# Optimization experiments

Hardware: AMD Instinct MI355X
Metric: run time of the kernel (lower is better)

The kernel has to match this reference:

```python
import jax, jax.numpy as jnp
import numpy as np
from jax import lax

B, W, K = 64, 128, 64      # batch, window_size, n_features
KS = 7                      # conv kernel size
EF = W                      # feature-attn embed dim (defaults to window_size, GATv1)
ET = 2 * K                  # temporal-attn embed dim (n_features doubled by GATv2)
H = 256                     # GRU hidden
FH = 256                    # forecast MLP hidden
ALPHA = 0.2                 # leaky relu slope


def _leaky(v):
    return jnp.where(v >= 0, v, ALPHA * v)


def setup_inputs() -> dict:
    key = jax.random.key(0)
    ks = jax.random.split(key, 20)
    s = 0.05
    inp = {
        "x": jax.random.normal(ks[0], (B, W, K), jnp.float32),
        # ConvLayer
        "conv_w": jax.random.normal(ks[1], (K, K, KS), jnp.float32) * s,
        "conv_b": jnp.zeros((K,), jnp.float32),
        # FeatureAttentionLayer (GATv1): lin W->EF, a:[2EF,1], bias [K,K]
        "feat_lin_w": jax.random.normal(ks[2], (EF, W), jnp.float32) * s,
        "feat_lin_b": jnp.zeros((EF,), jnp.float32),
        "feat_a": jax.random.normal(ks[3], (2 * EF, 1), jnp.float32) * s,
        "feat_bias": jnp.zeros((K, K), jnp.float32),
        # TemporalAttentionLayer (GATv2): lin 2K->ET, a:[ET,1], bias [W,W]
        "temp_lin_w": jax.random.normal(ks[4], (ET, 2 * K), jnp.float32) * s,
        "temp_lin_b": jnp.zeros((ET,), jnp.float32),
        "temp_a": jax.random.normal(ks[5], (ET, 1), jnp.float32) * s,
        "temp_bias": jnp.zeros((W, W), jnp.float32),
        # GRU (1 layer), input dim 3K
        "gru_wih": jax.random.normal(ks[6], (3 * H, 3 * K), jnp.float32) * s,
        "gru_whh": jax.random.normal(ks[7], (3 * H, H), jnp.float32) * s,
        "gru_bih": jnp.zeros((3 * H,), jnp.float32),
        "gru_bhh": jnp.zeros((3 * H,), jnp.float32),
        "fc0_w": jax.random.normal(ks[8], (FH, H), jnp.float32) * s,
        "fc0_b": jnp.zeros((FH,), jnp.float32),
        "fc1_w": jax.random.normal(ks[9], (FH, FH), jnp.float32) * s,
        "fc1_b": jnp.zeros((FH,), jnp.float32),
        "fc2_w": jax.random.normal(ks[10], (FH, FH), jnp.float32) * s,
        "fc2_b": jnp.zeros((FH,), jnp.float32),
        "fc3_w": jax.random.normal(ks[11], (K, FH), jnp.float32) * s,
        "fc3_b": jnp.zeros((K,), jnp.float32),
    }
    return inp


def _forward(x, conv_w, conv_b, feat_lin_w, feat_lin_b, feat_a, feat_bias,
             temp_lin_w, temp_lin_b, temp_a, temp_bias,
             gru_wih, gru_whh, gru_bih, gru_bhh,
             fc0_w, fc0_b, fc1_w, fc1_b, fc2_w, fc2_b, fc3_w, fc3_b):
    # --- ConvLayer: pad (k-1)//2 both sides, Conv1d K->K, ReLU ---
    pad = (KS - 1) // 2
    xc = x.transpose(0, 2, 1)                                   # [B,K,W]
    xc = jnp.pad(xc, ((0, 0), (0, 0), (pad, pad)))
    y = lax.conv_general_dilated(xc, conv_w, (1,), 'VALID',
                                 dimension_numbers=('NCH', 'OIH', 'NCH'))
    y = jax.nn.relu(y + conv_b[None, :, None]).transpose(0, 2, 1)  # [B,W,K]

    # --- FeatureAttentionLayer (GATv1): e_ij = leaky((Wx_i||Wx_j)·a) ---
    xf = y.transpose(0, 2, 1)                                   # [B,K,W]
    Wx = xf @ feat_lin_w.T + feat_lin_b                         # [B,K,EF]
    s1 = Wx @ feat_a[:EF, 0]                                    # [B,K]
    s2 = Wx @ feat_a[EF:, 0]                                    # [B,K]
    e_f = _leaky(s1[:, :, None] + s2[:, None, :]) + feat_bias   # [B,K,K]
    att_f = jax.nn.softmax(e_f, axis=2)
    h_feat = jax.nn.sigmoid(att_f @ xf).transpose(0, 2, 1)      # [B,W,K]

    # --- TemporalAttentionLayer (GATv2): g = leaky(lin(x_i||x_j)); e = g·a ---
    W1, W2 = temp_lin_w[:, :K], temp_lin_w[:, K:]               # split lin over concat halves
    p = y @ W1.T                                                # [B,W,ET]
    q = y @ W2.T                                                # [B,W,ET]
    g = _leaky(p[:, :, None, :] + q[:, None, :, :] + temp_lin_b)  # [B,W,W,ET]
    e_t = (g @ temp_a)[..., 0] + temp_bias                      # [B,W,W]
    att_t = jax.nn.softmax(e_t, axis=2)
    h_temp = jax.nn.sigmoid(att_t @ y)                          # [B,W,K]

    # --- concat + GRU over time ---
    z = jnp.concatenate([y, h_feat, h_temp], axis=2)            # [B,W,3K]

    def gru_step(h, xt):
        gi = xt @ gru_wih.T + gru_bih                           # [B,3H]
        gh = h @ gru_whh.T + gru_bhh
        ir, iz, inn = jnp.split(gi, 3, axis=1)
        hr, hz, hn = jnp.split(gh, 3, axis=1)
        r = jax.nn.sigmoid(ir + hr)
        zg = jax.nn.sigmoid(iz + hz)
        n = jnp.tanh(inn + r * hn)
        return (1.0 - zg) * n + zg * h, None

    h0 = jnp.zeros((z.shape[0], H), z.dtype)
    h_end, _ = lax.scan(gru_step, h0, z.transpose(1, 0, 2))     # [B,H]

    # --- Forecasting MLP (eval mode: dropout is identity) ---
    v = jax.nn.relu(h_end @ fc0_w.T + fc0_b)
    v = jax.nn.relu(v @ fc1_w.T + fc1_b)
    v = jax.nn.relu(v @ fc2_w.T + fc2_b)
    return v @ fc3_w.T + fc3_b                                  # [B,K]


def reference(x, conv_w, conv_b, feat_lin_w, feat_lin_b, feat_a, feat_bias,
              temp_lin_w, temp_lin_b, temp_a, temp_bias,
              gru_wih, gru_whh, gru_bih, gru_bhh,
              fc0_w, fc0_b, fc1_w, fc1_b, fc2_w, fc2_b, fc3_w, fc3_b):
    return _forward(x, conv_w, conv_b, feat_lin_w, feat_lin_b, feat_a, feat_bias,
                    temp_lin_w, temp_lin_b, temp_a, temp_bias,
                    gru_wih, gru_whh, gru_bih, gru_bhh,
                    fc0_w, fc0_b, fc1_w, fc1_b, fc2_w, fc2_b, fc3_w, fc3_b)
```

## Files before the change

### kernel.cpp

```cpp
#include <hip/hip_runtime.h>
#include <hip/hip_bf16.h>

typedef unsigned int uint;
typedef _Float16 half2_t __attribute__((ext_vector_type(2)));

union H2U { uint u; half2_t h; };

#if defined(__has_builtin)
#if __has_builtin(__builtin_amdgcn_fdot2)
#define HAVE_FDOT2 1
#endif
#endif

__device__ __forceinline__ float dot2acc(uint w, uint hh, float acc) {
    H2U a; a.u = w; H2U b; b.u = hh;
#ifdef HAVE_FDOT2
    return __builtin_amdgcn_fdot2(a.h, b.h, acc, false);
#else
    return acc + (float)a.h.x * (float)b.h.x + (float)a.h.y * (float)b.h.y;
#endif
}

#define OFF_Y    0u
#define OFF_Z    524288u
#define OFF_GI   2097152u
#define OFF_WHH  8388608u
#define OFF_C12  8486912u
#define OFF_DD   8487168u
#define OFF_HEND 8487424u

__global__ void k_prep(const float* __restrict__ flw, const float* __restrict__ flb,
                       const float* __restrict__ fa, float* __restrict__ c12,
                       float* __restrict__ dd) {
    int tid = threadIdx.x;
    float a = 0.f, b = 0.f;
    for (int e = 0; e < 128; ++e) {
        float w = flw[e * 128 + tid];
        a = fmaf(w, fa[e], a);
        b = fmaf(w, fa[128 + e], b);
    }
    c12[tid] = a;
    c12[128 + tid] = b;
    if (tid == 0) {
        float d1 = 0.f, d2 = 0.f;
        for (int e = 0; e < 128; ++e) { d1 += flb[e] * fa[e]; d2 += flb[e] * fa[128 + e]; }
        dd[0] = d1; dd[1] = d2;
    }
}

__global__ __launch_bounds__(256) void k_pack(const float* __restrict__ whh, uint* __restrict__ w16) {
    int idx = blockIdx.x * 256 + threadIdx.x;
    if (idx >= 98304) return;
    int tidq = idx >> 7;
    int r7 = idx & 127;
    int rowpar = r7 >> 6;
    int i = r7 & 63;
    int half = tidq / 384;
    int m = tidq % 384;
    int row = 2 * m + rowpar;
    int pc = half * 64 + i;
    float a = whh[(size_t)row * 256 + 2 * pc];
    float b = whh[(size_t)row * 256 + 2 * pc + 1];
    H2U u; u.h.x = (_Float16)a; u.h.y = (_Float16)b;
    w16[idx] = u.u;
}

__global__ __launch_bounds__(256) void k_conv(const float* __restrict__ x, const float* __restrict__ cw,
                                              const float* __restrict__ cb, float* __restrict__ y,
                                              float* __restrict__ z) {
    __shared__ float xT[64][41];
    __shared__ float cwL[64 * 64 * 7];
    int b = blockIdx.y, w0 = blockIdx.x * 32, tid = threadIdx.x;
    for (int idx = tid; idx < 38 * 64; idx += 256) {
        int wl = idx / 64, k = idx % 64;
        int wg = w0 - 3 + wl;
        xT[k][wl] = (wg >= 0 && wg < 128) ? x[((size_t)b * 128 + wg) * 64 + k] : 0.f;
    }
    for (int idx = tid; idx < 64 * 64 * 7; idx += 256) cwL[idx] = cw[idx];
    __syncthreads();
    int w_l = tid % 32, kog = tid / 32;
    float acc[8];
#pragma unroll
    for (int i = 0; i < 8; ++i) acc[i] = 0.f;
    for (int ki = 0; ki < 64; ++ki) {
        float x7[7];
#pragma unroll
        for (int u = 0; u < 7; ++u) x7[u] = xT[ki][w_l + u];
#pragma unroll
        for (int koi = 0; koi < 8; ++koi) {
            const float* wp = &cwL[((kog * 8 + koi) * 64 + ki) * 7];
#pragma unroll
            for (int u = 0; u < 7; ++u) acc[koi] = fmaf(x7[u], wp[u], acc[koi]);
        }
    }
    int w = w0 + w_l;
#pragma unroll
    for (int koi = 0; koi < 8; ++koi) {
        int ko = kog * 8 + koi;
        float v = acc[koi] + cb[ko];
        v = v > 0.f ? v : 0.f;
        y[((size_t)b * 128 + w) * 64 + ko] = v;
        z[((size_t)b * 128 + w) * 192 + ko] = v;
    }
}

__global__ __launch_bounds__(256) void k_feat(const float* __restrict__ y, const float* __restrict__ c12,
                                              const float* __restrict__ dd, const float* __restrict__ fb,
                                              float* __restrict__ z) {
    int b = blockIdx.y, w0 = blockIdx.x * 32, tid = threadIdx.x;
    __shared__ float s1L[64], s2L[64];
    __shared__ float attL[64][65];
    __shared__ float yL[32][64];
    __shared__ float cL[256];
    cL[tid] = c12[tid];
    for (int idx = tid; idx < 32 * 64; idx += 256) {
        int wl = idx / 64, j = idx % 64;
        yL[wl][j] = y[((size_t)b * 128 + w0 + wl) * 64 + j];
    }
    __syncthreads();
    if (tid < 128) {
        int k = tid % 64;
        const float* c = (tid < 64) ? cL : cL + 128;
        float acc = 0.f;
        for (int w = 0; w < 128; ++w) acc = fmaf(y[((size_t)b * 128 + w) * 64 + k], c[w], acc);
        if (tid < 64) s1L[k] = acc + dd[0]; else s2L[k] = acc + dd[1];
    }
    __syncthreads();
    if (tid < 64) {
        int k = tid;
        float s1 = s1L[k];
        float m = -1e30f;
        for (int j = 0; j < 64; ++j) {
            float v = s1 + s2L[j];
            float l = fmaxf(v, 0.2f * v);
            float e = l + fb[k * 64 + j];
            attL[k][j] = e;
            m = fmaxf(m, e);
        }
        float s = 0.f;
        for (int j = 0; j < 64; ++j) { float e = __expf(attL[k][j] - m); attL[k][j] = e; s += e; }
        float inv = 1.f / s;
        for (int j = 0; j < 64; ++j) attL[k][j] *= inv;
    }
    __syncthreads();
    int k_l = tid % 64, wg = tid / 64;
    for (int wi = 0; wi < 8; ++wi) {
        int wl = wg * 8 + wi;
        float acc = 0.f;
#pragma unroll 16
        for (int j = 0; j < 64; ++j) acc = fmaf(attL[k_l][j], yL[wl][j], acc);
        float hv = 1.f / (1.f + __expf(-acc));
        z[((size_t)b * 128 + w0 + wl) * 192 + 64 + k_l] = hv;
    }
}

__global__ __launch_bounds__(512) void k_temp(const float* __restrict__ y, const float* __restrict__ tlw,
                                              const float* __restrict__ tlb, const float* __restrict__ ta,
                                              const float* __restrict__ tbias, float* __restrict__ z) {
    int b = blockIdx.y, i0 = blockIdx.x * 32, tid = threadIdx.x;
    __shared__ __align__(16) float yT[64][132];
    __shared__ __align__(16) float qL[128][128];
    __shared__ __align__(16) float pL[32][128];
    __shared__ __align__(16) float etL[32][128];
    __shared__ __align__(16) float taL[128];
    __shared__ float mred[32][8], sred[32][8];
    __shared__ float mrow[32], invL[32];
    if (tid < 128) taL[tid] = ta[tid];
    for (int idx = tid; idx < 8192; idx += 512) {
        int j = idx >> 6, k = idx & 63;
        yT[k][j] = y[((size_t)b * 128 + j) * 64 + k];
    }
    __syncthreads();
    {
        int c = tid & 127, ih = tid >> 7;
        float w1r[64];
        const float4* w1p = (const float4*)(tlw + c * 128);
#pragma unroll
        for (int q4 = 0; q4 < 16; ++q4) {
            float4 v = w1p[q4];
            w1r[4 * q4] = v.x; w1r[4 * q4 + 1] = v.y; w1r[4 * q4 + 2] = v.z; w1r[4 * q4 + 3] = v.w;
        }
        float base = tlb[c];
#pragma unroll
        for (int ilb = 0; ilb < 2; ++ilb) {
            int j0 = i0 + ih * 8 + ilb * 4;
            float4 acc = {base, base, base, base};
            for (int k = 0; k < 64; ++k) {
                float4 yv = *((const float4*)&yT[k][j0]);
                float w = w1r[k];
                acc.x = fmaf(yv.x, w, acc.x); acc.y = fmaf(yv.y, w, acc.y);
                acc.z = fmaf(yv.z, w, acc.z); acc.w = fmaf(yv.w, w, acc.w);
            }
            int il = ih * 8 + ilb * 4;
            pL[il][c] = acc.x; pL[il + 1][c] = acc.y; pL[il + 2][c] = acc.z; pL[il + 3][c] = acc.w;
        }
    }
    {
        int j = tid & 127, ch = tid >> 7;
        float yreg[64];
#pragma unroll
        for (int k = 0; k < 64; ++k) yreg[k] = yT[k][j];
        for (int cc = 0; cc < 32; ++cc) {
            int c = __builtin_amdgcn_readfirstlane(ch * 32 + cc);
            const float* w2 = tlw + c * 128 + 64;
            float acc = 0.f;
#pragma unroll
            for (int k = 0; k < 64; ++k) acc = fmaf(yreg[k], w2[k], acc);
            qL[c][j] = acc;
        }
    }
    __syncthreads();
    {
        int jg = tid & 31, ih = tid >> 5;
        int j0 = jg * 4;
        int il0 = ih * 2;
        float4 acc0 = *((const float4*)(tbias + (size_t)(i0 + il0) * 128 + j0));
        float4 acc1 = *((const float4*)(tbias + (size_t)(i0 + il0 + 1) * 128 + j0));
        for (int c0 = 0; c0 < 128; c0 += 4) {
            float4 ta4 = *((const float4*)&taL[c0]);
            float4 p0 = *((const float4*)&pL[il0][c0]);
            float4 p1 = *((const float4*)&pL[il0 + 1][c0]);
            float4 q0 = *((const float4*)&qL[c0 + 0][j0]);
            float4 q1 = *((const float4*)&qL[c0 + 1][j0]);
            float4 q2 = *((const float4*)&qL[c0 + 2][j0]);
            float4 q3 = *((const float4*)&qL[c0 + 3][j0]);
#define ETSTEP(qv, tac, pa, pb) { \
            float u; \
            u = (pa) + qv.x; acc0.x = fmaf(fmaxf(u, 0.2f * u), (tac), acc0.x); \
            u = (pa) + qv.y; acc0.y = fmaf(fmaxf(u, 0.2f * u), (tac), acc0.y); \
            u = (pa) + qv.z; acc0.z = fmaf(fmaxf(u, 0.2f * u), (tac), acc0.z); \
            u = (pa) + qv.w; acc0.w = fmaf(fmaxf(u, 0.2f * u), (tac), acc0.w); \
            u = (pb) + qv.x; acc1.x = fmaf(fmaxf(u, 0.2f * u), (tac), acc1.x); \
            u = (pb) + qv.y; acc1.y = fmaf(fmaxf(u, 0.2f * u), (tac), acc1.y); \
            u = (pb) + qv.z; acc1.z = fmaf(fmaxf(u, 0.2f * u), (tac), acc1.z); \
            u = (pb) + qv.w; acc1.w = fmaf(fmaxf(u, 0.2f * u), (tac), acc1.w); }
            ETSTEP(q0, ta4.x, p0.x, p1.x)
            ETSTEP(q1, ta4.y, p0.y, p1.y)
            ETSTEP(q2, ta4.z, p0.z, p1.z)
            ETSTEP(q3, ta4.w, p0.w, p1.w)
#undef ETSTEP
        }
        *((float4*)&etL[il0][j0]) = acc0;
        *((float4*)&etL[il0 + 1][j0]) = acc1;
    }
    __syncthreads();
    if (tid < 256) {
        int il = tid >> 3, seg = tid & 7;
        const float4* ep = (const float4*)&etL[il][seg * 16];
        float m = -1e30f;
#pragma unroll
        for (int q = 0; q < 4; ++q) {
            float4 e = ep[q];
            m = fmaxf(m, fmaxf(fmaxf(e.x, e.y), fmaxf(e.z, e.w)));
        }
        mred[il][seg] = m;
    }
    __syncthreads();
    if (tid < 32) {
        float m = mred[tid][0];
#pragma unroll
        for (int s = 1; s < 8; ++s) m = fmaxf(m, mred[tid][s]);
        mrow[tid] = m;
    }
    __syncthreads();
    if (tid < 256) {
        int il = tid >> 3, seg = tid & 7;
        float m = mrow[il];
        float4* ep = (float4*)&etL[il][seg * 16];
        float s = 0.f;
#pragma unroll
        for (int q = 0; q < 4; ++q) {
            float4 e = ep[q];
            e.x = __expf(e.x - m); e.y = __expf(e.y - m);
            e.z = __expf(e.z - m); e.w = __expf(e.w - m);
            s += (e.x + e.y) + (e.z + e.w);
            ep[q] = e;
        }
        sred[il][seg] = s;
    }
    __syncthreads();
    if (tid < 32) {
        float s = 0.f;
#pragma unroll
        for (int q = 0; q < 8; ++q) s += sred[tid][q];
        invL[tid] = 1.f / s;
    }
    __syncthreads();
    {
        int k = tid & 63, ig = tid >> 6;
        float acc[4] = {0.f, 0.f, 0.f, 0.f};
        const float* yb = y + (size_t)b * 128 * 64 + k;
        for (int j0 = 0; j0 < 128; j0 += 4) {
            float yv[4];
#pragma unroll
            for (int jj = 0; jj < 4; ++jj) yv[jj] = yb[(size_t)(j0 + jj) * 64];
#pragma unroll
            for (int ii = 0; ii < 4; ++ii) {
                int il = ig * 4 + ii;
                float4 ev = *((const float4*)&etL[il][j0]);
                acc[ii] = fmaf(ev.x, yv[0], acc[ii]);
                acc[ii] = fmaf(ev.y, yv[1], acc[ii]);
                acc[ii] = fmaf(ev.z, yv[2], acc[ii]);
                acc[ii] = fmaf(ev.w, yv[3], acc[ii]);
            }
        }
#pragma unroll
        for (int ii = 0; ii < 4; ++ii) {
            int il = ig * 4 + ii;
            float hv = 1.f / (1.f + __expf(-acc[ii] * invL[il]));
            z[((size_t)b * 128 + i0 + il) * 192 + 128 + k] = hv;
        }
    }
}

__global__ __launch_bounds__(256) void k_gi(const float* __restrict__ z, const float* __restrict__ wih,
                                            const float* __restrict__ bih, float* __restrict__ gi) {
    int o0 = blockIdx.x * 128;
    int bt0 = blockIdx.y * 64;
    int tid = threadIdx.x;
    int o_l = tid % 128, rg = tid / 128;
    __shared__ float zL[64][64];
    __shared__ float wT[64][133];
    float acc[32];
#pragma unroll
    for (int r = 0; r < 32; ++r) acc[r] = 0.f;
    for (int mc = 0; mc < 3; ++mc) {
        int m0 = mc * 64;
        __syncthreads();
        for (int idx = tid; idx < 64 * 64; idx += 256) {
            int r = idx / 64, mm = idx % 64;
            zL[r][mm] = z[(size_t)(bt0 + r) * 192 + m0 + mm];
        }
        for (int idx = tid; idx < 128 * 64; idx += 256) {
            int o = idx / 64, mm = idx % 64;
            wT[mm][o] = wih[(size_t)(o0 + o) * 192 + m0 + mm];
        }
        __syncthreads();
        for (int mm = 0; mm < 64; ++mm) {
            float w = wT[mm][o_l];
#pragma unroll
            for (int r = 0; r < 32; ++r) acc[r] = fmaf(zL[rg * 32 + r][mm], w, acc[r]);
        }
    }
    float bo = bih[o0 + o_l];
#pragma unroll
    for (int r = 0; r < 32; ++r)
        gi[(size_t)(bt0 + rg * 32 + r) * 768 + o0 + o_l] = acc[r] + bo;
}

__global__ __launch_bounds__(768, 3) void k_gru(const float* __restrict__ gi,
                                                const uint* __restrict__ w16,
                                                const float* __restrict__ bhh,
                                                float* __restrict__ hend) {
    int b = blockIdx.x, tid = threadIdx.x;
    int m = tid % 384, half = tid / 384;
    int t = tid & 255;
    __shared__ __align__(16) uint4 hp4s[32];
    __shared__ float sH[2][768];
    uint4 wv[32];
    {
        const uint4* wp = (const uint4*)(w16 + (size_t)tid * 128);
#pragma unroll
        for (int i = 0; i < 32; ++i) wv[i] = wp[i];
    }
    float br = 0.f, bz = 0.f, bn = 0.f;
    if (tid < 256) { br = bhh[t]; bz = bhh[256 + t]; bn = bhh[512 + t]; }
    float h = 0.f;
    if (tid < 32) { uint4 zz; zz.x = zz.y = zz.z = zz.w = 0u; hp4s[tid] = zz; }
    __syncthreads();
    const float* gib = gi + (size_t)b * 128 * 768;
    const uint4* hbase = hp4s + half * 16;
    for (int s = 0; s < 128; ++s) {
        float gr = 0.f, gz = 0.f, gn = 0.f;
        if (tid < 256) {
            gr = gib[s * 768 + t];
            gz = gib[s * 768 + 256 + t];
            gn = gib[s * 768 + 512 + t];
        }
        float a0 = 0.f, a1 = 0.f, c0 = 0.f, c1 = 0.f;
#pragma unroll
        for (int j = 0; j < 16; ++j) {
            uint4 hv = hbase[j];
            uint4 wa = wv[j];
            uint4 wb = wv[16 + j];
            a0 = dot2acc(wa.x, hv.x, a0); a1 = dot2acc(wa.y, hv.y, a1);
            a0 = dot2acc(wa.z, hv.z, a0); a1 = dot2acc(wa.w, hv.w, a1);
            c0 = dot2acc(wb.x, hv.x, c0); c1 = dot2acc(wb.y, hv.y, c1);
            c0 = dot2acc(wb.z, hv.z, c0); c1 = dot2acc(wb.w, hv.w, c1);
        }
        float2 pr; pr.x = a0 + a1; pr.y = c0 + c1;
        *((float2*)&sH[half][2 * m]) = pr;
        __syncthreads();
        if (tid < 256) {
            float hr = sH[0][t] + sH[1][t] + br;
            float hz = sH[0][256 + t] + sH[1][256 + t] + bz;
            float hn = sH[0][512 + t] + sH[1][512 + t] + bn;
            float r  = 1.f / (1.f + __expf(-(gr + hr)));
            float zg = 1.f / (1.f + __expf(-(gz + hz)));
            float nx = gn + r * hn;
            float n  = 1.f - 2.f / (1.f + __expf(2.f * nx));
            h = (1.f - zg) * n + zg * h;
            ((_Float16*)hp4s)[t] = (_Float16)h;
        }
        __syncthreads();
    }
    if (tid < 256) hend[b * 256 + t] = h;
}

__global__ __launch_bounds__(256) void k_fc(const float* __restrict__ hend,
                                            const float* __restrict__ w0, const float* __restrict__ b0,
                                            const float* __restrict__ w1, const float* __restrict__ b1,
                                            const float* __restrict__ w2, const float* __restrict__ b2,
                                            const float* __restrict__ w3, const float* __restrict__ b3,
                                            float* __restrict__ out) {
    int b = blockIdx.x, tid = threadIdx.x;
    __shared__ float bufA[256], bufB[256];
    bufA[tid] = hend[b * 256 + tid];
    __syncthreads();
    {
        float acc = b0[tid];
        const float* wrow = &w0[tid * 256];
#pragma unroll 8
        for (int m = 0; m < 256; ++m) acc = fmaf(wrow[m], bufA[m], acc);
        bufB[tid] = fmaxf(acc, 0.f);
    }
    __syncthreads();
    {
        float acc = b1[tid];
        const float* wrow = &w1[tid * 256];
#pragma unroll 8
        for (int m = 0; m < 256; ++m) acc = fmaf(wrow[m], bufB[m], acc);
        bufA[tid] = fmaxf(acc, 0.f);
    }
    __syncthreads();
    {
        float acc = b2[tid];
        const float* wrow = &w2[tid * 256];
#pragma unroll 8
        for (int m = 0; m < 256; ++m) acc = fmaf(wrow[m], bufA[m], acc);
        bufB[tid] = fmaxf(acc, 0.f);
    }
    __syncthreads();
    if (tid < 64) {
        float acc = b3[tid];
        const float* wrow = &w3[tid * 256];
#pragma unroll 8
        for (int m = 0; m < 256; ++m) acc = fmaf(wrow[m], bufB[m], acc);
        out[b * 64 + tid] = acc;
    }
}

extern "C" void kernel_launch(void* const* d_in, const int* in_sizes, int n_in,
                              void* d_out, int out_size, void* d_ws, size_t ws_size,
                              hipStream_t stream) {
    const float* x    = (const float*)d_in[0];
    const float* cw   = (const float*)d_in[1];
    const float* cb   = (const float*)d_in[2];
    const float* flw  = (const float*)d_in[3];
    const float* flb  = (const float*)d_in[4];
    const float* fa   = (const float*)d_in[5];
    const float* fb   = (const float*)d_in[6];
    const float* tlw  = (const float*)d_in[7];
    const float* tlb  = (const float*)d_in[8];
    const float* ta   = (const float*)d_in[9];
    const float* tb   = (const float*)d_in[10];
    const float* wih  = (const float*)d_in[11];
    const float* whh  = (const float*)d_in[12];
    const float* bih  = (const float*)d_in[13];
    const float* bhh  = (const float*)d_in[14];
    const float* fc0w = (const float*)d_in[15];
    const float* fc0b = (const float*)d_in[16];
    const float* fc1w = (const float*)d_in[17];
    const float* fc1b = (const float*)d_in[18];
    const float* fc2w = (const float*)d_in[19];
    const float* fc2b = (const float*)d_in[20];
    const float* fc3w = (const float*)d_in[21];
    const float* fc3b = (const float*)d_in[22];

    float* wsf  = (float*)d_ws;
    float* y    = wsf + OFF_Y;
    float* z    = wsf + OFF_Z;
    float* gi   = wsf + OFF_GI;
    uint*  w16  = (uint*)(wsf + OFF_WHH);
    float* c12  = wsf + OFF_C12;
    float* dd   = wsf + OFF_DD;
    float* hend = wsf + OFF_HEND;
    float* out  = (float*)d_out;

    k_prep<<<1, 128, 0, stream>>>(flw, flb, fa, c12, dd);
    k_pack<<<384, 256, 0, stream>>>(whh, w16);
    k_conv<<<dim3(4, 64), 256, 0, stream>>>(x, cw, cb, y, z);
    k_feat<<<dim3(4, 64), 256, 0, stream>>>(y, c12, dd, fb, z);
    k_temp<<<dim3(4, 64), 512, 0, stream>>>(y, tlw, tlb, ta, tb, z);
    k_gi<<<dim3(6, 128), 256, 0, stream>>>(z, wih, bih, gi);
    k_gru<<<64, 768, 0, stream>>>(gi, w16, bhh, hend);
    k_fc<<<64, 256, 0, stream>>>(hend, fc0w, fc0b, fc1w, fc1b, fc2w, fc2b, fc3w, fc3b, out);
}
```

Before: 459.6 us.

## Restructure GRU to 512 threads with 3 rows each, register-tile gi GEMM, merge prep

The GRU recurrence kernel now uses 512 threads per block, each holding three rows of fp16-packed W_hh in registers (pinned with empty asm constraints), instead of 768 threads with two rows each. This cuts the number of waves taking part in each per-step barrier and gives every hidden-state LDS read more reuse. The input-gate GEMM is rewritten as an 8x4 register-blocked tile with float4 global loads, and the weight-pack and feature-prep kernels are merged into one launch. Register pressure in the GRU rises to about 192 VGPRs for weights, so spilling is a risk.

```diff
diff --git a/kernel.cpp b/kernel.cpp
--- a/kernel.cpp
+++ b/kernel.cpp
@@ -29,40 +29,46 @@
 #define OFF_DD   8487168u
 #define OFF_HEND 8487424u
 
-__global__ void k_prep(const float* __restrict__ flw, const float* __restrict__ flb,
-                       const float* __restrict__ fa, float* __restrict__ c12,
-                       float* __restrict__ dd) {
-    int tid = threadIdx.x;
-    float a = 0.f, b = 0.f;
-    for (int e = 0; e < 128; ++e) {
-        float w = flw[e * 128 + tid];
-        a = fmaf(w, fa[e], a);
-        b = fmaf(w, fa[128 + e], b);
-    }
-    c12[tid] = a;
-    c12[128 + tid] = b;
-    if (tid == 0) {
-        float d1 = 0.f, d2 = 0.f;
-        for (int e = 0; e < 128; ++e) { d1 += flb[e] * fa[e]; d2 += flb[e] * fa[128 + e]; }
-        dd[0] = d1; dd[1] = d2;
-    }
-}
-
-__global__ __launch_bounds__(256) void k_pack(const float* __restrict__ whh, uint* __restrict__ w16) {
-    int idx = blockIdx.x * 256 + threadIdx.x;
-    if (idx >= 98304) return;
-    int tidq = idx >> 7;
-    int r7 = idx & 127;
-    int rowpar = r7 >> 6;
-    int i = r7 & 63;
-    int half = tidq / 384;
-    int m = tidq % 384;
-    int row = 2 * m + rowpar;
-    int pc = half * 64 + i;
-    float a = whh[(size_t)row * 256 + 2 * pc];
-    float b = whh[(size_t)row * 256 + 2 * pc + 1];
-    H2U u; u.h.x = (_Float16)a; u.h.y = (_Float16)b;
-    w16[idx] = u.u;
+__global__ __launch_bounds__(256) void k_pack_prep(const float* __restrict__ whh, uint* __restrict__ w16,
+                                                   const float* __restrict__ flw, const float* __restrict__ flb,
+                                                   const float* __restrict__ fa, float* __restrict__ c12,
+                                                   float* __restrict__ dd) {
+    __shared__ float red[256];
+    int bx = blockIdx.x, tid = threadIdx.x;
+    if (bx < 384) {
+        int idx = bx * 256 + tid;
+        int tidq = idx / 192;
+        int rem = idx - tidq * 192;
+        int rp = rem >> 6;
+        int i = rem & 63;
+        int half = tidq >> 8;
+        int mloc = tidq & 255;
+        int row = 3 * mloc + rp;
+        int pc = half * 64 + i;
+        float a = whh[(size_t)row * 256 + 2 * pc];
+        float b = whh[(size_t)row * 256 + 2 * pc + 1];
+        H2U u; u.h.x = (_Float16)a; u.h.y = (_Float16)b;
+        w16[idx] = u.u;
+    } else {
+        if (tid < 128) {
+            float a = 0.f, b = 0.f;
+            for (int e = 0; e < 128; ++e) {
+                float w = flw[e * 128 + tid];
+                a = fmaf(w, fa[e], a);
+                b = fmaf(w, fa[128 + e], b);
+            }
+            c12[tid] = a;
+            c12[128 + tid] = b;
+        }
+        int e = tid & 127;
+        red[tid] = (tid < 128) ? flb[e] * fa[e] : flb[e] * fa[128 + e];
+        __syncthreads();
+        if (tid < 2) {
+            float s = 0.f;
+            for (int q = 0; q < 128; ++q) s += red[tid * 128 + q];
+            dd[tid] = s;
+        }
+    }
 }
 
 __global__ __launch_bounds__(256) void k_conv(const float* __restrict__ x, const float* __restrict__ cw,
@@ -318,51 +324,97 @@
     int o0 = blockIdx.x * 128;
     int bt0 = blockIdx.y * 64;
     int tid = threadIdx.x;
-    int o_l = tid % 128, rg = tid / 128;
-    __shared__ float zL[64][64];
-    __shared__ float wT[64][133];
-    float acc[32];
-#pragma unroll
-    for (int r = 0; r < 32; ++r) acc[r] = 0.f;
+    __shared__ __align__(16) float zL[64][68];
+    __shared__ float wL[128][65];
+    int ol = tid & 31;
+    int r8 = (tid >> 5) * 8;
+    float acc[8][4];
+#pragma unroll
+    for (int rr = 0; rr < 8; ++rr)
+#pragma unroll
+        for (int oo = 0; oo < 4; ++oo) acc[rr][oo] = 0.f;
     for (int mc = 0; mc < 3; ++mc) {
         int m0 = mc * 64;
         __syncthreads();
-        for (int idx = tid; idx < 64 * 64; idx += 256) {
-            int r = idx / 64, mm = idx % 64;
-            zL[r][mm] = z[(size_t)(bt0 + r) * 192 + m0 + mm];
-        }
-        for (int idx = tid; idx < 128 * 64; idx += 256) {
-            int o = idx / 64, mm = idx % 64;
-            wT[mm][o] = wih[(size_t)(o0 + o) * 192 + m0 + mm];
+        {
+            int mq = (tid & 15) * 4;
+            int r = tid >> 4;
+#pragma unroll
+            for (int it = 0; it < 4; ++it, r += 16) {
+                float4 v = *((const float4*)&z[(size_t)(bt0 + r) * 192 + m0 + mq]);
+                *((float4*)&zL[r][mq]) = v;
+            }
+            int o = tid >> 4;
+#pragma unroll
+            for (int it = 0; it < 8; ++it, o += 16) {
+                float4 v = *((const float4*)&wih[(size_t)(o0 + o) * 192 + m0 + mq]);
+                wL[o][mq] = v.x; wL[o][mq + 1] = v.y; wL[o][mq + 2] = v.z; wL[o][mq + 3] = v.w;
+            }
         }
         __syncthreads();
-        for (int mm = 0; mm < 64; ++mm) {
-            float w = wT[mm][o_l];
-#pragma unroll
-            for (int r = 0; r < 32; ++r) acc[r] = fmaf(zL[rg * 32 + r][mm], w, acc[r]);
-        }
-    }
-    float bo = bih[o0 + o_l];
-#pragma unroll
-    for (int r = 0; r < 32; ++r)
-        gi[(size_t)(bt0 + rg * 32 + r) * 768 + o0 + o_l] = acc[r] + bo;
-}
-
-__global__ __launch_bounds__(768, 3) void k_gru(const float* __restrict__ gi,
+        for (int mb = 0; mb < 64; mb += 4) {
+            float4 zv[8];
+#pragma unroll
+            for (int rr = 0; rr < 8; ++rr) zv[rr] = *((const float4*)&zL[r8 + rr][mb]);
+#pragma unroll
+            for (int mi = 0; mi < 4; ++mi) {
+                float wv[4];
+#pragma unroll
+                for (int oo = 0; oo < 4; ++oo) wv[oo] = wL[ol + 32 * oo][mb + mi];
+#pragma unroll
+                for (int rr = 0; rr < 8; ++rr) {
+                    float zc = (mi == 0) ? zv[rr].x : (mi == 1) ? zv[rr].y : (mi == 2) ? zv[rr].z : zv[rr].w;
+#pragma unroll
+                    for (int oo = 0; oo < 4; ++oo) acc[rr][oo] = fmaf(zc, wv[oo], acc[rr][oo]);
+                }
+            }
+        }
+    }
+    float bo[4];
+#pragma unroll
+    for (int oo = 0; oo < 4; ++oo) bo[oo] = bih[o0 + ol + 32 * oo];
+#pragma unroll
+    for (int rr = 0; rr < 8; ++rr)
+#pragma unroll
+        for (int oo = 0; oo < 4; ++oo)
+            gi[(size_t)(bt0 + r8 + rr) * 768 + o0 + ol + 32 * oo] = acc[rr][oo] + bo[oo];
+}
+
+#define KEEP4(W) asm volatile("" : "+v"(W.x), "+v"(W.y), "+v"(W.z), "+v"(W.w))
+__global__ __launch_bounds__(512, 2) void k_gru(const float* __restrict__ gi,
                                                 const uint* __restrict__ w16,
                                                 const float* __restrict__ bhh,
                                                 float* __restrict__ hend) {
     int b = blockIdx.x, tid = threadIdx.x;
-    int m = tid % 384, half = tid / 384;
+    int half = tid >> 8, mloc = tid & 255;
     int t = tid & 255;
     __shared__ __align__(16) uint4 hp4s[32];
     __shared__ float sH[2][768];
-    uint4 wv[32];
-    {
-        const uint4* wp = (const uint4*)(w16 + (size_t)tid * 128);
-#pragma unroll
-        for (int i = 0; i < 32; ++i) wv[i] = wp[i];
-    }
+    const uint4* wp = (const uint4*)(w16 + (size_t)tid * 192);
+    uint4 wa0 = wp[0],  wa1 = wp[1],  wa2 = wp[2],  wa3 = wp[3];
+    uint4 wa4 = wp[4],  wa5 = wp[5],  wa6 = wp[6],  wa7 = wp[7];
+    uint4 wa8 = wp[8],  wa9 = wp[9],  wa10 = wp[10], wa11 = wp[11];
+    uint4 wa12 = wp[12], wa13 = wp[13], wa14 = wp[14], wa15 = wp[15];
+    uint4 wb0 = wp[16], wb1 = wp[17], wb2 = wp[18], wb3 = wp[19];
+    uint4 wb4 = wp[20], wb5 = wp[21], wb6 = wp[22], wb7 = wp[23];
+    uint4 wb8 = wp[24], wb9 = wp[25], wb10 = wp[26], wb11 = wp[27];
+    uint4 wb12 = wp[28], wb13 = wp[29], wb14 = wp[30], wb15 = wp[31];
+    uint4 wc0 = wp[32], wc1 = wp[33], wc2 = wp[34], wc3 = wp[35];
+    uint4 wc4 = wp[36], wc5 = wp[37], wc6 = wp[38], wc7 = wp[39];
+    uint4 wc8 = wp[40], wc9 = wp[41], wc10 = wp[42], wc11 = wp[43];
+    uint4 wc12 = wp[44], wc13 = wp[45], wc14 = wp[46], wc15 = wp[47];
+    KEEP4(wa0); KEEP4(wa1); KEEP4(wa2); KEEP4(wa3);
+    KEEP4(wa4); KEEP4(wa5); KEEP4(wa6); KEEP4(wa7);
+    KEEP4(wa8); KEEP4(wa9); KEEP4(wa10); KEEP4(wa11);
+    KEEP4(wa12); KEEP4(wa13); KEEP4(wa14); KEEP4(wa15);
+    KEEP4(wb0); KEEP4(wb1); KEEP4(wb2); KEEP4(wb3);
+    KEEP4(wb4); KEEP4(wb5); KEEP4(wb6); KEEP4(wb7);
+    KEEP4(wb8); KEEP4(wb9); KEEP4(wb10); KEEP4(wb11);
+    KEEP4(wb12); KEEP4(wb13); KEEP4(wb14); KEEP4(wb15);
+    KEEP4(wc0); KEEP4(wc1); KEEP4(wc2); KEEP4(wc3);
+    KEEP4(wc4); KEEP4(wc5); KEEP4(wc6); KEEP4(wc7);
+    KEEP4(wc8); KEEP4(wc9); KEEP4(wc10); KEEP4(wc11);
+    KEEP4(wc12); KEEP4(wc13); KEEP4(wc14); KEEP4(wc15);
     float br = 0.f, bz = 0.f, bn = 0.f;
     if (tid < 256) { br = bhh[t]; bz = bhh[256 + t]; bn = bhh[512 + t]; }
     float h = 0.f;
@@ -370,6 +422,7 @@
     __syncthreads();
     const float* gib = gi + (size_t)b * 128 * 768;
     const uint4* hbase = hp4s + half * 16;
+    int m3 = 3 * mloc;
     for (int s = 0; s < 128; ++s) {
         float gr = 0.f, gz = 0.f, gn = 0.f;
         if (tid < 256) {
@@ -377,19 +430,26 @@
             gz = gib[s * 768 + 256 + t];
             gn = gib[s * 768 + 512 + t];
         }
-        float a0 = 0.f, a1 = 0.f, c0 = 0.f, c1 = 0.f;
-#pragma unroll
-        for (int j = 0; j < 16; ++j) {
-            uint4 hv = hbase[j];
-            uint4 wa = wv[j];
-            uint4 wb = wv[16 + j];
-            a0 = dot2acc(wa.x, hv.x, a0); a1 = dot2acc(wa.y, hv.y, a1);
-            a0 = dot2acc(wa.z, hv.z, a0); a1 = dot2acc(wa.w, hv.w, a1);
-            c0 = dot2acc(wb.x, hv.x, c0); c1 = dot2acc(wb.y, hv.y, c1);
-            c0 = dot2acc(wb.z, hv.z, c0); c1 = dot2acc(wb.w, hv.w, c1);
-        }
-        float2 pr; pr.x = a0 + a1; pr.y = c0 + c1;
-        *((float2*)&sH[half][2 * m]) = pr;
+        float a0 = 0.f, a1 = 0.f, b0 = 0.f, b1 = 0.f, c0 = 0.f, c1 = 0.f;
+#define GSTEP(J, WA, WB, WC) { uint4 hv = hbase[J]; \
+        a0 = dot2acc(WA.x, hv.x, a0); a1 = dot2acc(WA.y, hv.y, a1); \
+        a0 = dot2acc(WA.z, hv.z, a0); a1 = dot2acc(WA.w, hv.w, a1); \
+        b0 = dot2acc(WB.x, hv.x, b0); b1 = dot2acc(WB.y, hv.y, b1); \
+        b0 = dot2acc(WB.z, hv.z, b0); b1 = dot2acc(WB.w, hv.w, b1); \
+        c0 = dot2acc(WC.x, hv.x, c0); c1 = dot2acc(WC.y, hv.y, c1); \
+        c0 = dot2acc(WC.z, hv.z, c0); c1 = dot2acc(WC.w, hv.w, c1); }
+        GSTEP(0, wa0, wb0, wc0)   GSTEP(1, wa1, wb1, wc1)
+        GSTEP(2, wa2, wb2, wc2)   GSTEP(3, wa3, wb3, wc3)
+        GSTEP(4, wa4, wb4, wc4)   GSTEP(5, wa5, wb5, wc5)
+        GSTEP(6, wa6, wb6, wc6)   GSTEP(7, wa7, wb7, wc7)
+        GSTEP(8, wa8, wb8, wc8)   GSTEP(9, wa9, wb9, wc9)
+        GSTEP(10, wa10, wb10, wc10) GSTEP(11, wa11, wb11, wc11)
+        GSTEP(12, wa12, wb12, wc12) GSTEP(13, wa13, wb13, wc13)
+        GSTEP(14, wa14, wb14, wc14) GSTEP(15, wa15, wb15, wc15)
+#undef GSTEP
+        sH[half][m3 + 0] = a0 + a1;
+        sH[half][m3 + 1] = b0 + b1;
+        sH[half][m3 + 2] = c0 + c1;
         __syncthreads();
         if (tid < 256) {
             float hr = sH[0][t] + sH[1][t] + br;
@@ -487,12 +547,11 @@
     float* hend = wsf + OFF_HEND;
     float* out  = (float*)d_out;
 
-    k_prep<<<1, 128, 0, stream>>>(flw, flb, fa, c12, dd);
-    k_pack<<<384, 256, 0, stream>>>(whh, w16);
+    k_pack_prep<<<385, 256, 0, stream>>>(whh, w16, flw, flb, fa, c12, dd);
     k_conv<<<dim3(4, 64), 256, 0, stream>>>(x, cw, cb, y, z);
     k_feat<<<dim3(4, 64), 256, 0, stream>>>(y, c12, dd, fb, z);
     k_temp<<<dim3(4, 64), 512, 0, stream>>>(y, tlw, tlb, ta, tb, z);
     k_gi<<<dim3(6, 128), 256, 0, stream>>>(z, wih, bih, gi);
-    k_gru<<<64, 768, 0, stream>>>(gi, w16, bhh, hend);
+    k_gru<<<64, 512, 0, stream>>>(gi, w16, bhh, hend);
     k_fc<<<64, 256, 0, stream>>>(hend, fc0w, fc0b, fc1w, fc1b, fc2w, fc2b, fc3w, fc3b, out);
 }
```

Result: faster. 417.0 us (-9.3%).
